# Optimization experiments

Measured on AMD Instinct MI355X. Metric: run time of the kernel, lower is better.

## Reference

```python
import jax, jax.numpy as jnp
import numpy as np
from jax import lax

B = 16           # graphs per batch
N_PER = 4096     # points per graph (equal-sized graphs)
C_IN = 32        # in_channels
RATIO = 0.25
MAX_NBR = 32     # max_num_neighbors in radius()


def _xavier(key, fan_in, fan_out):
    lim = np.sqrt(6.0 / (fan_in + fan_out)).astype(np.float32)
    return jax.random.uniform(key, (fan_in, fan_out), jnp.float32, -lim, lim)


def setup_inputs() -> dict:
    key = jax.random.key(0)
    ks = jax.random.split(key, 16)
    x = jax.random.normal(ks[0], (B * N_PER, C_IN), jnp.float32)
    pos = jax.random.uniform(ks[1], (B * N_PER, 3), jnp.float32) * 20.0
    batch = jnp.repeat(jnp.arange(B, dtype=jnp.int64), N_PER)
    p = {
        'x': x, 'pos': pos, 'batch': batch,
        'scaler_mean': jnp.zeros((1, C_IN), jnp.float32),
        'scaler_std': jnp.ones((1, C_IN), jnp.float32),
        # SA1: Linear(32+3,64) -> Sigmoid -> Linear(64,128)
        'sa1_w1': _xavier(ks[2], C_IN + 3, 64), 'sa1_b1': jnp.zeros((64,), jnp.float32),
        'sa1_w2': _xavier(ks[3], 64, 128),      'sa1_b2': jnp.zeros((128,), jnp.float32),
        # SA2: Linear(128+3,128) -> Sigmoid -> Linear(128,256)
        'sa2_w1': _xavier(ks[4], 128 + 3, 128), 'sa2_b1': jnp.zeros((128,), jnp.float32),
        'sa2_w2': _xavier(ks[5], 128, 256),     'sa2_b2': jnp.zeros((256,), jnp.float32),
        # Global SA: Linear(256+3,256) -> Sigmoid -> Linear(256,512)
        'g_w1': _xavier(ks[6], 256 + 3, 256),   'g_b1': jnp.zeros((256,), jnp.float32),
        'g_w2': _xavier(ks[7], 256, 512),       'g_b2': jnp.zeros((512,), jnp.float32),
        # fc: Linear(512,256) -> Sigmoid -> Linear(256,128)
        'fc_w1': _xavier(ks[8], 512, 256),      'fc_b1': jnp.zeros((256,), jnp.float32),
        'fc_w2': _xavier(ks[9], 256, 128),      'fc_b2': jnp.zeros((128,), jnp.float32),
    }
    return p


def _fps(pos, k):
    # Farthest point sampling, deterministic start at index 0. pos: [B, n, 3] -> idx [B, k]
    pos = lax.stop_gradient(pos)
    d0 = jnp.sum((pos - pos[:, :1, :]) ** 2, -1)  # [B, n] dist^2 to start point

    def step(mind, _):
        nxt = jnp.argmax(mind, axis=1)                                  # [B]
        p = jnp.take_along_axis(pos, nxt[:, None, None], axis=1)        # [B,1,3]
        mind = jnp.minimum(mind, jnp.sum((pos - p) ** 2, -1))
        return mind, nxt

    _, rest = lax.scan(step, d0, None, length=k - 1)                    # [k-1, B]
    start = jnp.zeros((1, pos.shape[0]), rest.dtype)
    return jnp.concatenate([start, rest], 0).T                          # [B, k]


def _gather_nbr(v, nbr):
    # v: [B, n, C], nbr: [B, k, MAX_NBR] -> [B, k, MAX_NBR, C]
    return jax.vmap(lambda vb, nb: vb[nb])(v, nbr)


def _sa_module(x, pos, w1, b1, w2, b2, ratio, r):
    # PointNetConv (max aggregation) over a radius graph from FPS centers.
    Bb, n, _ = x.shape
    k = int(n * ratio)
    idx = _fps(pos, k)                                                  # [B, k]
    pos_dst = jnp.take_along_axis(pos, idx[:, :, None], axis=1)         # [B, k, 3]
    d2 = jnp.sum((pos_dst[:, :, None, :] - pos[:, None, :, :]) ** 2, -1)  # [B,k,n]
    masked = jnp.where(d2 <= r * r, d2, jnp.inf)
    negv, nbr = lax.top_k(-masked, MAX_NBR)                             # nearest <=32 within radius
    valid = jnp.isfinite(negv)                                          # [B,k,32]
    x_j = _gather_nbr(x, nbr)                                           # [B,k,32,C]
    rel = _gather_nbr(pos, nbr) - pos_dst[:, :, None, :]                # pos_j - pos_i
    feat = jnp.concatenate([x_j, rel], axis=-1)
    msg = jax.nn.sigmoid(feat @ w1 + b1) @ w2 + b2                      # [B,k,32,2h]
    msg = jnp.where(valid[..., None], msg, -jnp.inf)
    agg = jnp.max(msg, axis=2)                                          # max aggregation
    agg = jnp.where(jnp.isfinite(agg), agg, 0.0)  # (self is always a neighbor, defensive)
    return jax.nn.relu(agg), pos_dst


def reference(x, pos, batch, scaler_mean, scaler_std,
              sa1_w1, sa1_b1, sa1_w2, sa1_b2,
              sa2_w1, sa2_b1, sa2_w2, sa2_b2,
              g_w1, g_b1, g_w2, g_b2,
              fc_w1, fc_b1, fc_w2, fc_b2):
    x = (x - scaler_mean) / scaler_std
    xb = x.reshape(B, N_PER, -1)      # batch is sorted with N_PER points per graph
    pb = pos.reshape(B, N_PER, 3)
    xb, pb = _sa_module(xb, pb, sa1_w1, sa1_b1, sa1_w2, sa1_b2, RATIO, 2.0)
    xb, pb = _sa_module(xb, pb, sa2_w1, sa2_b1, sa2_w2, sa2_b2, RATIO, 4.0)
    # GlobalSAModule: relu(nn(cat[x, pos])) then global max pool
    h = jnp.concatenate([xb, pb], axis=-1)
    h = jax.nn.relu(jax.nn.sigmoid(h @ g_w1 + g_b1) @ g_w2 + g_b2)      # [B, 256, 512]
    g = jnp.max(h, axis=1)                                              # [B, 512]
    out = jax.nn.sigmoid(g @ fc_w1 + fc_b1) @ fc_w2 + fc_b2
    return jax.nn.relu(out)                                             # last_act='relu'
```

## Files before the change

kernel.cpp:

```cpp
#include <hip/hip_runtime.h>
#include <hip/hip_bf16.h>
#include <math.h>

namespace {

constexpr int NB   = 16;
constexpr int N1   = 4096;
constexpr int K1   = 1024;
constexpr int K2   = 256;
constexpr int MAXN = 32;

__device__ __forceinline__ float sigmoidf_(float x) {
  return 1.0f / (1.0f + __expf(-x));
}

__device__ __forceinline__ float readlane_f(float v, int l) {
  return __int_as_float(__builtin_amdgcn_readlane(__float_as_int(v), l));
}


#define FPS_DPP_STEP(CTRL)                                                     \
  {                                                                            \
    const unsigned olo =                                                       \
        (unsigned)__builtin_amdgcn_update_dpp(0, (int)lo, (CTRL), 0xF, 0xF, true); \
    const unsigned ohi =                                                       \
        (unsigned)__builtin_amdgcn_update_dpp(0, (int)hi, (CTRL), 0xF, 0xF, true); \
    const unsigned long long o = ((unsigned long long)ohi << 32) | olo;        \
    const unsigned long long cur = ((unsigned long long)hi << 32) | lo;        \
    if (o > cur) { lo = olo; hi = ohi; }                                       \
  }

template<int NPT>
__device__ __forceinline__ void fps_level(
    const float* __restrict__ sx, const float* __restrict__ sy,
    const float* __restrict__ sz, int k,
    float* __restrict__ selx, float* __restrict__ sely,
    float* __restrict__ selz,
    unsigned long long (*red)[4]) {
  const int t = threadIdx.x;
  const int lane = t & 63, wave = t >> 6;
  float px[NPT], py[NPT], pz[NPT], mind[NPT];
  unsigned niv[NPT];
  const float c0x = sx[0], c0y = sy[0], c0z = sz[0];
  unsigned long long best = 0;
#pragma unroll
  for (int i = 0; i < NPT; i++) {
    const int p = i * 256 + t;
    niv[i] = ~(unsigned)p;
    px[i] = sx[p]; py[i] = sy[p]; pz[i] = sz[p];
    const float dx = px[i] - c0x, dy = py[i] - c0y, dz = pz[i] - c0z;
    const float d2 = dx * dx + dy * dy + dz * dz;
    mind[i] = d2;
    const unsigned long long cand =
        ((unsigned long long)__float_as_uint(d2) << 32) | niv[i];
    if (cand > best) best = cand;
  }
  if (t == 0) { selx[0] = c0x; sely[0] = c0y; selz[0] = c0z; }
  for (int it = 1; it < k; it++) {
    unsigned lo = (unsigned)best, hi = (unsigned)(best >> 32);
    FPS_DPP_STEP(0x111)
    FPS_DPP_STEP(0x112)
    FPS_DPP_STEP(0x114)
    FPS_DPP_STEP(0x118)
    FPS_DPP_STEP(0x142)
    FPS_DPP_STEP(0x143)
    const int par = it & 1;
    if (lane == 63) red[par][wave] = ((unsigned long long)hi << 32) | lo;
    __syncthreads();
    const unsigned long long w0 = red[par][0], w1 = red[par][1];
    const unsigned long long w2 = red[par][2], w3 = red[par][3];
    const unsigned long long m01 = w0 > w1 ? w0 : w1;
    const unsigned long long m23 = w2 > w3 ? w2 : w3;
    const unsigned long long win = m01 > m23 ? m01 : m23;
    const int p = (int)(~(unsigned)win);
    const float nx = sx[p], ny = sy[p], nz = sz[p];
    if (t == 0) { selx[it] = nx; sely[it] = ny; selz[it] = nz; }
    best = 0;
#pragma unroll
    for (int i = 0; i < NPT; i++) {
      const float dx = px[i] - nx, dy = py[i] - ny, dz = pz[i] - nz;
      const float d2 = dx * dx + dy * dy + dz * dz;
      const float m = fminf(mind[i], d2);
      mind[i] = m;
      const unsigned long long cand =
          ((unsigned long long)__float_as_uint(m) << 32) | niv[i];
      if (cand > best) best = cand;
    }
  }
}

#undef FPS_DPP_STEP

__global__ __launch_bounds__(256) void fps_fused_kernel(
    const float* __restrict__ pos, float* __restrict__ posd1,
    float* __restrict__ posd2, unsigned int* __restrict__ gout) {
  __shared__ float sx[N1], sy[N1], sz[N1];
  __shared__ float s2x[K1], s2y[K1], s2z[K1];
  __shared__ float p2x[K2], p2y[K2], p2z[K2];
  __shared__ __align__(16) unsigned long long red[2][4];
  const int b = blockIdx.x;
  const int t = threadIdx.x;
  gout[b * 512 + t] = 0u;
  gout[b * 512 + t + 256] = 0u;
  const float* pb = pos + (size_t)b * N1 * 3;
  for (int p = t; p < N1; p += 256) {
    sx[p] = pb[p * 3 + 0]; sy[p] = pb[p * 3 + 1]; sz[p] = pb[p * 3 + 2];
  }
  __syncthreads();
  fps_level<N1 / 256>(sx, sy, sz, K1, s2x, s2y, s2z, red);
  __syncthreads();
  fps_level<K1 / 256>(s2x, s2y, s2z, K2, p2x, p2y, p2z, red);
  __syncthreads();
  float* o1 = posd1 + (size_t)b * K1 * 3;
  for (int i = t; i < K1; i += 256) {
    o1[i * 3 + 0] = s2x[i]; o1[i * 3 + 1] = s2y[i]; o1[i * 3 + 2] = s2z[i];
  }
  float* o2 = posd2 + (size_t)b * K2 * 3;
  for (int i = t; i < K2; i += 256) {
    o2[i * 3 + 0] = p2x[i]; o2[i * 3 + 1] = p2y[i]; o2[i * 3 + 2] = p2z[i];
  }
}

template<int N, int CAP>
__global__ __launch_bounds__(256) void radius_nbr_kernel(
    const float* __restrict__ pts, const float* __restrict__ ctr,
    int K, float r2, int* __restrict__ nbr, int* __restrict__ cnt_out) {
  __shared__ float candd[4][CAP];
  __shared__ int   candi[4][CAP];
  const int t = threadIdx.x;
  const int lane = t & 63, wave = t >> 6;
  const int bpg = K / 4;
  const int b = blockIdx.x / bpg;
  const int ci = (blockIdx.x % bpg) * 4 + wave;
  const float* pb = pts + (size_t)b * N * 3;
  const size_t cbase = ((size_t)b * K + ci) * 3;
  const float cx = ctr[cbase + 0], cy = ctr[cbase + 1], cz = ctr[cbase + 2];
  int total = 0;
  for (int base = 0; base < N; base += 64) {
    const int p = base + lane;
    const float dx = pb[p * 3 + 0] - cx;
    const float dy = pb[p * 3 + 1] - cy;
    const float dz = pb[p * 3 + 2] - cz;
    const float d2 = dx * dx + dy * dy + dz * dz;
    const bool pred = d2 <= r2;
    const unsigned long long m = __ballot(pred);
    if (pred) {
      const int slot = total + __popcll(m & ((1ull << lane) - 1ull));
      if (slot < CAP) { candd[wave][slot] = d2; candi[wave][slot] = p; }
    }
    total += __popcll(m);
  }
  if (total > CAP) total = CAP;
  int* nbp = nbr + ((size_t)b * K + ci) * MAXN;
  if (total <= MAXN) {
    if (lane < total) nbp[lane] = candi[wave][lane];
  } else {
    for (int jj = 0; jj < MAXN; jj++) {
      float bvd = INFINITY; int bvi = 0x7fffffff; int bslot = 0;
      for (int s = lane; s < total; s += 64) {
        const float d = candd[wave][s];
        const int i = candi[wave][s];
        if (d < bvd || (d == bvd && i < bvi)) { bvd = d; bvi = i; bslot = s; }
      }
#pragma unroll
      for (int off = 32; off; off >>= 1) {
        const float od = __shfl_xor(bvd, off);
        const int   oi = __shfl_xor(bvi, off);
        const int   os = __shfl_xor(bslot, off);
        if (od < bvd || (od == bvd && oi < bvi)) { bvd = od; bvi = oi; bslot = os; }
      }
      if (lane == 0) { nbp[jj] = bvi; candd[wave][bslot] = INFINITY; }
    }
  }
  if (lane == 0) cnt_out[(size_t)b * K + ci] = (total < MAXN) ? total : MAXN;
}

template<int CIN_T, int H, int COUT, bool SCALE>
__global__ __launch_bounds__(256) void sa_conv_kernel(
    const float* __restrict__ xin, const float* __restrict__ pts,
    const float* __restrict__ ctr, const int* __restrict__ nbr,
    const int* __restrict__ cnt,
    const float* __restrict__ w1, const float* __restrict__ b1,
    const float* __restrict__ w2, const float* __restrict__ b2,
    const float* __restrict__ smean, const float* __restrict__ sstd,
    int N, int K, float* __restrict__ xout) {
  constexpr int FIN  = CIN_T + 3;
  constexpr int KREG = (FIN + 63) / 64;
  constexpr int HREG = H / 64;
  constexpr int CREG = COUT / 64;
  constexpr int RPW  = MAXN / 4;
  __shared__ float part[4][COUT];
  const int t = threadIdx.x, lane = t & 63, wave = t >> 6;
  const int bk = blockIdx.x;
  const int b = bk / K;
  const int V = cnt[bk];
  float m[CREG];
#pragma unroll
  for (int ck = 0; ck < CREG; ck++) m[ck] = -INFINITY;
  if (V > wave * RPW) {
    const int* nb = nbr + (size_t)bk * MAXN;
    const float ctrx = ctr[(size_t)bk * 3 + 0];
    const float ctry = ctr[(size_t)bk * 3 + 1];
    const float ctrz = ctr[(size_t)bk * 3 + 2];
    float sm = 0.0f, sd = 1.0f;
    if (SCALE && lane < CIN_T) { sm = smean[lane]; sd = sstd[lane]; }
    float fr[RPW][KREG];
#pragma unroll
    for (int r = 0; r < RPW; r++) {
      const int j = wave * RPW + r;
      const int p = (j < V) ? nb[j] : nb[0];
#pragma unroll
      for (int k2 = 0; k2 < KREG; k2++) {
        const int f = k2 * 64 + lane;
        float v = 0.0f;
        if (f < CIN_T) {
          v = xin[((size_t)b * N + p) * CIN_T + f];
          if constexpr (SCALE) v = (v - sm) / sd;
        } else if (f < FIN) {
          const int d = f - CIN_T;
          const float pv = pts[((size_t)b * N + p) * 3 + d];
          v = pv - (d == 0 ? ctrx : (d == 1 ? ctry : ctrz));
        }
        fr[r][k2] = v;
      }
    }
    float hh[RPW][HREG];
    {
      float acc[RPW][HREG];
#pragma unroll
      for (int r = 0; r < RPW; r++)
#pragma unroll
        for (int hk = 0; hk < HREG; hk++) acc[r][hk] = 0.0f;
#pragma unroll
      for (int k2 = 0; k2 < KREG; k2++) {
        const int lim = (FIN - k2 * 64) < 64 ? (FIN - k2 * 64) : 64;
        for (int fl = 0; fl < lim; fl++) {
          const int f = k2 * 64 + fl;
          float wv[HREG];
#pragma unroll
          for (int hk = 0; hk < HREG; hk++) wv[hk] = w1[(size_t)f * H + hk * 64 + lane];
#pragma unroll
          for (int r = 0; r < RPW; r++) {
            const float s = readlane_f(fr[r][k2], fl);
#pragma unroll
            for (int hk = 0; hk < HREG; hk++) acc[r][hk] = fmaf(s, wv[hk], acc[r][hk]);
          }
        }
      }
#pragma unroll
      for (int hk = 0; hk < HREG; hk++) {
        const float bb = b1[hk * 64 + lane];
#pragma unroll
        for (int r = 0; r < RPW; r++) hh[r][hk] = sigmoidf_(acc[r][hk] + bb);
      }
    }
    float acc2[RPW][CREG];
#pragma unroll
    for (int r = 0; r < RPW; r++)
#pragma unroll
      for (int ck = 0; ck < CREG; ck++) acc2[r][ck] = 0.0f;
#pragma unroll
    for (int hk = 0; hk < HREG; hk++) {
      for (int hl = 0; hl < 64; hl++) {
        const int h = hk * 64 + hl;
        float wv[CREG];
#pragma unroll
        for (int ck = 0; ck < CREG; ck++) wv[ck] = w2[(size_t)h * COUT + ck * 64 + lane];
#pragma unroll
        for (int r = 0; r < RPW; r++) {
          const float s = readlane_f(hh[r][hk], hl);
#pragma unroll
          for (int ck = 0; ck < CREG; ck++) acc2[r][ck] = fmaf(s, wv[ck], acc2[r][ck]);
        }
      }
    }
#pragma unroll
    for (int r = 0; r < RPW; r++) {
      if (wave * RPW + r < V) {
#pragma unroll
        for (int ck = 0; ck < CREG; ck++) m[ck] = fmaxf(m[ck], acc2[r][ck]);
      }
    }
  }
#pragma unroll
  for (int ck = 0; ck < CREG; ck++) part[wave][ck * 64 + lane] = m[ck];
  __syncthreads();
  if (t < COUT) {
    const float mm = fmaxf(fmaxf(part[0][t], part[1][t]),
                           fmaxf(part[2][t], part[3][t]));
    const float o = mm + b2[t];
    xout[(size_t)bk * COUT + t] = o > 0.0f ? o : 0.0f;
  }
}

__global__ __launch_bounds__(256) void global_sa_kernel(
    const float* __restrict__ x2, const float* __restrict__ posd2,
    const float* __restrict__ gw1, const float* __restrict__ gb1,
    const float* __restrict__ gw2, const float* __restrict__ gb2,
    unsigned int* __restrict__ gout) {
  __shared__ float fin[4][259];
  __shared__ float s[4][256];
  const int t = threadIdx.x;
  const int blk = blockIdx.x;
  const int b = blk / 64;
  const int p0 = (blk % 64) * 4;
  for (int item = t; item < 4 * 259; item += 256) {
    const int p = item / 259, f = item - p * 259;
    const float v = (f < 256)
        ? x2[((size_t)b * 256 + p0 + p) * 256 + f]
        : posd2[((size_t)b * 256 + p0 + p) * 3 + (f - 256)];
    fin[p][f] = v;
  }
  __syncthreads();
  float acc[4] = {0.f, 0.f, 0.f, 0.f};
  for (int f = 0; f < 259; f++) {
    const float w = gw1[f * 256 + t];
#pragma unroll
    for (int p = 0; p < 4; p++) acc[p] = fmaf(fin[p][f], w, acc[p]);
  }
  const float bb = gb1[t];
#pragma unroll
  for (int p = 0; p < 4; p++) s[p][t] = sigmoidf_(acc[p] + bb);
  __syncthreads();
  float a0[4] = {0.f, 0.f, 0.f, 0.f}, a1[4] = {0.f, 0.f, 0.f, 0.f};
  for (int h = 0; h < 256; h++) {
    const float w0 = gw2[h * 512 + t];
    const float w1v = gw2[h * 512 + t + 256];
#pragma unroll
    for (int p = 0; p < 4; p++) {
      a0[p] = fmaf(s[p][h], w0, a0[p]);
      a1[p] = fmaf(s[p][h], w1v, a1[p]);
    }
  }
  const float b0 = gb2[t], b1v = gb2[t + 256];
  float m0 = 0.0f, m1 = 0.0f;
#pragma unroll
  for (int p = 0; p < 4; p++) {
    m0 = fmaxf(m0, fmaxf(a0[p] + b0, 0.0f));
    m1 = fmaxf(m1, fmaxf(a1[p] + b1v, 0.0f));
  }
  atomicMax(&gout[b * 512 + t], __float_as_uint(m0));
  atomicMax(&gout[b * 512 + t + 256], __float_as_uint(m1));
}

__global__ __launch_bounds__(256) void fc_kernel(
    const unsigned int* __restrict__ g,
    const float* __restrict__ fw1, const float* __restrict__ fb1,
    const float* __restrict__ fw2, const float* __restrict__ fb2,
    float* __restrict__ out) {
  __shared__ float gv[512];
  __shared__ float s[256];
  const int b = blockIdx.x, t = threadIdx.x;
  gv[t] = __uint_as_float(g[b * 512 + t]);
  gv[t + 256] = __uint_as_float(g[b * 512 + t + 256]);
  __syncthreads();
  float acc = 0.0f;
  for (int h = 0; h < 512; h++) acc = fmaf(gv[h], fw1[h * 256 + t], acc);
  s[t] = sigmoidf_(acc + fb1[t]);
  __syncthreads();
  if (t < 128) {
    float a2 = 0.0f;
    for (int h = 0; h < 256; h++) a2 = fmaf(s[h], fw2[h * 128 + t], a2);
    const float o = a2 + fb2[t];
    out[b * 128 + t] = o > 0.0f ? o : 0.0f;
  }
}

}

extern "C" void kernel_launch(void* const* d_in, const int* in_sizes, int n_in,
                              void* d_out, int out_size, void* d_ws, size_t ws_size,
                              hipStream_t stream) {
  (void)in_sizes; (void)n_in; (void)out_size; (void)ws_size;
  const float* x     = (const float*)d_in[0];
  const float* pos   = (const float*)d_in[1];
  const float* smean = (const float*)d_in[3];
  const float* sstd  = (const float*)d_in[4];
  const float* s1w1  = (const float*)d_in[5];
  const float* s1b1  = (const float*)d_in[6];
  const float* s1w2  = (const float*)d_in[7];
  const float* s1b2  = (const float*)d_in[8];
  const float* s2w1  = (const float*)d_in[9];
  const float* s2b1  = (const float*)d_in[10];
  const float* s2w2  = (const float*)d_in[11];
  const float* s2b2  = (const float*)d_in[12];
  const float* gw1   = (const float*)d_in[13];
  const float* gb1   = (const float*)d_in[14];
  const float* gw2   = (const float*)d_in[15];
  const float* gb2   = (const float*)d_in[16];
  const float* fw1   = (const float*)d_in[17];
  const float* fb1   = (const float*)d_in[18];
  const float* fw2   = (const float*)d_in[19];
  const float* fb2   = (const float*)d_in[20];

  char* ws = (char*)d_ws;
  size_t off = 0;
  auto take = [&](size_t bytes) -> char* {
    char* p = ws + off;
    off = (off + bytes + 255) & ~(size_t)255;
    return p;
  };
  float* posd1       = (float*)take((size_t)NB * K1 * 3 * 4);
  int*   nbr1        = (int*)take((size_t)NB * K1 * MAXN * 4);
  int*   cnt1        = (int*)take((size_t)NB * K1 * 4);
  float* x1          = (float*)take((size_t)NB * K1 * 128 * 4);
  float* posd2       = (float*)take((size_t)NB * K2 * 3 * 4);
  int*   nbr2        = (int*)take((size_t)NB * K2 * MAXN * 4);
  int*   cnt2        = (int*)take((size_t)NB * K2 * 4);
  float* x2          = (float*)take((size_t)NB * K2 * 256 * 4);
  unsigned int* gbuf = (unsigned int*)take((size_t)NB * 512 * 4);

  hipLaunchKernelGGL(fps_fused_kernel, dim3(NB), dim3(256), 0, stream,
                     pos, posd1, posd2, gbuf);
  hipLaunchKernelGGL((radius_nbr_kernel<N1, 448>), dim3(NB * K1 / 4), dim3(256), 0, stream,
                     pos, posd1, K1, 4.0f, nbr1, cnt1);
  hipLaunchKernelGGL((sa_conv_kernel<32, 64, 128, true>), dim3(NB * K1), dim3(256), 0, stream,
                     x, pos, posd1, nbr1, cnt1, s1w1, s1b1, s1w2, s1b2,
                     smean, sstd, N1, K1, x1);
  hipLaunchKernelGGL((radius_nbr_kernel<K1, 448>), dim3(NB * K2 / 4), dim3(256), 0, stream,
                     posd1, posd2, K2, 16.0f, nbr2, cnt2);
  hipLaunchKernelGGL((sa_conv_kernel<128, 128, 256, false>), dim3(NB * K2), dim3(256), 0, stream,
                     x1, posd1, posd2, nbr2, cnt2, s2w1, s2b1, s2w2, s2b2,
                     nullptr, nullptr, K1, K2, x2);
  hipLaunchKernelGGL(global_sa_kernel, dim3(NB * 64), dim3(256), 0, stream,
                     x2, posd2, gw1, gb1, gw2, gb2, gbuf);
  hipLaunchKernelGGL(fc_kernel, dim3(NB), dim3(256), 0, stream,
                     gbuf, fw1, fb1, fw2, fb2, (float*)d_out);
}
```

Baseline: 1.275 ms.

## Split FPS levels and co-schedule independent stages in merged heterogeneous kernels

Second-level farthest point sampling moves out of the single-block-per-graph FPS kernel into a merged kernel that also runs the level-1 radius search, so the serial FPS runs alongside the radius blocks. Likewise, the level-2 radius search and the level-1 SA conv share one launch, since neither depends on the other. The SA conv weight loads also change to vectorized float2/float4 with an interleaved channel mapping per lane. The aim is to hide the long-latency, 16-block serial FPS behind parallel work and cut launch gaps. The cost is larger shared-memory footprints on the merged kernels, which may lower occupancy.

```diff
diff --git a/kernel.cpp b/kernel.cpp
--- a/kernel.cpp
+++ b/kernel.cpp
@@ -9,6 +9,7 @@
 constexpr int K1   = 1024;
 constexpr int K2   = 256;
 constexpr int MAXN = 32;
+constexpr int RCAP = 448;
 
 __device__ __forceinline__ float sigmoidf_(float x) {
   return 1.0f / (1.0f + __expf(-x));
@@ -91,12 +92,11 @@
 
 #undef FPS_DPP_STEP
 
-__global__ __launch_bounds__(256) void fps_fused_kernel(
+__global__ __launch_bounds__(256) void fps_l1_kernel(
     const float* __restrict__ pos, float* __restrict__ posd1,
-    float* __restrict__ posd2, unsigned int* __restrict__ gout) {
+    unsigned int* __restrict__ gout) {
   __shared__ float sx[N1], sy[N1], sz[N1];
   __shared__ float s2x[K1], s2y[K1], s2z[K1];
-  __shared__ float p2x[K2], p2y[K2], p2z[K2];
   __shared__ __align__(16) unsigned long long red[2][4];
   const int b = blockIdx.x;
   const int t = threadIdx.x;
@@ -109,29 +109,32 @@
   __syncthreads();
   fps_level<N1 / 256>(sx, sy, sz, K1, s2x, s2y, s2z, red);
   __syncthreads();
-  fps_level<K1 / 256>(s2x, s2y, s2z, K2, p2x, p2y, p2z, red);
-  __syncthreads();
   float* o1 = posd1 + (size_t)b * K1 * 3;
   for (int i = t; i < K1; i += 256) {
     o1[i * 3 + 0] = s2x[i]; o1[i * 3 + 1] = s2y[i]; o1[i * 3 + 2] = s2z[i];
   }
-  float* o2 = posd2 + (size_t)b * K2 * 3;
-  for (int i = t; i < K2; i += 256) {
-    o2[i * 3 + 0] = p2x[i]; o2[i * 3 + 1] = p2y[i]; o2[i * 3 + 2] = p2z[i];
-  }
-}
-
-template<int N, int CAP>
-__global__ __launch_bounds__(256) void radius_nbr_kernel(
+}
+
+struct FpsL2Smem {
+  float s2x[K1], s2y[K1], s2z[K1];
+  float p2x[K2], p2y[K2], p2z[K2];
+  unsigned long long red[2][4];
+};
+struct RadSmem {
+  float candd[4][RCAP];
+  int   candi[4][RCAP];
+};
+
+template<int N>
+__device__ __forceinline__ void radius_body(
     const float* __restrict__ pts, const float* __restrict__ ctr,
-    int K, float r2, int* __restrict__ nbr, int* __restrict__ cnt_out) {
-  __shared__ float candd[4][CAP];
-  __shared__ int   candi[4][CAP];
+    int K, float r2, int* __restrict__ nbr, int* __restrict__ cnt_out,
+    RadSmem& sm, int rb) {
   const int t = threadIdx.x;
   const int lane = t & 63, wave = t >> 6;
   const int bpg = K / 4;
-  const int b = blockIdx.x / bpg;
-  const int ci = (blockIdx.x % bpg) * 4 + wave;
+  const int b = rb / bpg;
+  const int ci = (rb % bpg) * 4 + wave;
   const float* pb = pts + (size_t)b * N * 3;
   const size_t cbase = ((size_t)b * K + ci) * 3;
   const float cx = ctr[cbase + 0], cy = ctr[cbase + 1], cz = ctr[cbase + 2];
@@ -146,20 +149,20 @@
     const unsigned long long m = __ballot(pred);
     if (pred) {
       const int slot = total + __popcll(m & ((1ull << lane) - 1ull));
-      if (slot < CAP) { candd[wave][slot] = d2; candi[wave][slot] = p; }
+      if (slot < RCAP) { sm.candd[wave][slot] = d2; sm.candi[wave][slot] = p; }
     }
     total += __popcll(m);
   }
-  if (total > CAP) total = CAP;
+  if (total > RCAP) total = RCAP;
   int* nbp = nbr + ((size_t)b * K + ci) * MAXN;
   if (total <= MAXN) {
-    if (lane < total) nbp[lane] = candi[wave][lane];
+    if (lane < total) nbp[lane] = sm.candi[wave][lane];
   } else {
     for (int jj = 0; jj < MAXN; jj++) {
       float bvd = INFINITY; int bvi = 0x7fffffff; int bslot = 0;
       for (int s = lane; s < total; s += 64) {
-        const float d = candd[wave][s];
-        const int i = candi[wave][s];
+        const float d = sm.candd[wave][s];
+        const int i = sm.candi[wave][s];
         if (d < bvd || (d == bvd && i < bvi)) { bvd = d; bvi = i; bslot = s; }
       }
 #pragma unroll
@@ -169,29 +172,56 @@
         const int   os = __shfl_xor(bslot, off);
         if (od < bvd || (od == bvd && oi < bvi)) { bvd = od; bvi = oi; bslot = os; }
       }
-      if (lane == 0) { nbp[jj] = bvi; candd[wave][bslot] = INFINITY; }
+      if (lane == 0) { nbp[jj] = bvi; sm.candd[wave][bslot] = INFINITY; }
     }
   }
   if (lane == 0) cnt_out[(size_t)b * K + ci] = (total < MAXN) ? total : MAXN;
 }
 
+__global__ __launch_bounds__(256) void l2_radius1_kernel(
+    const float* __restrict__ pos, const float* __restrict__ posd1,
+    float* __restrict__ posd2, int* __restrict__ nbr1,
+    int* __restrict__ cnt1) {
+  constexpr size_t SMB =
+      sizeof(FpsL2Smem) > sizeof(RadSmem) ? sizeof(FpsL2Smem) : sizeof(RadSmem);
+  __shared__ __align__(16) char smem[SMB];
+  const int t = threadIdx.x;
+  if (blockIdx.x < (unsigned)NB) {
+    FpsL2Smem& f = *reinterpret_cast<FpsL2Smem*>(smem);
+    const int b = blockIdx.x;
+    const float* p1 = posd1 + (size_t)b * K1 * 3;
+    for (int i = t; i < K1; i += 256) {
+      f.s2x[i] = p1[i * 3 + 0]; f.s2y[i] = p1[i * 3 + 1]; f.s2z[i] = p1[i * 3 + 2];
+    }
+    __syncthreads();
+    fps_level<K1 / 256>(f.s2x, f.s2y, f.s2z, K2, f.p2x, f.p2y, f.p2z, f.red);
+    __syncthreads();
+    float* o2 = posd2 + (size_t)b * K2 * 3;
+    for (int i = t; i < K2; i += 256) {
+      o2[i * 3 + 0] = f.p2x[i]; o2[i * 3 + 1] = f.p2y[i]; o2[i * 3 + 2] = f.p2z[i];
+    }
+  } else {
+    RadSmem& r = *reinterpret_cast<RadSmem*>(smem);
+    radius_body<N1>(pos, posd1, K1, 4.0f, nbr1, cnt1, r, blockIdx.x - NB);
+  }
+}
+
 template<int CIN_T, int H, int COUT, bool SCALE>
-__global__ __launch_bounds__(256) void sa_conv_kernel(
+__device__ __forceinline__ void sa_conv_body(
     const float* __restrict__ xin, const float* __restrict__ pts,
     const float* __restrict__ ctr, const int* __restrict__ nbr,
     const int* __restrict__ cnt,
     const float* __restrict__ w1, const float* __restrict__ b1,
     const float* __restrict__ w2, const float* __restrict__ b2,
     const float* __restrict__ smean, const float* __restrict__ sstd,
-    int N, int K, float* __restrict__ xout) {
+    int N, int K, float* __restrict__ xout, float* part ,
+    int bk) {
   constexpr int FIN  = CIN_T + 3;
   constexpr int KREG = (FIN + 63) / 64;
   constexpr int HREG = H / 64;
   constexpr int CREG = COUT / 64;
   constexpr int RPW  = MAXN / 4;
-  __shared__ float part[4][COUT];
   const int t = threadIdx.x, lane = t & 63, wave = t >> 6;
-  const int bk = blockIdx.x;
   const int b = bk / K;
   const int V = cnt[bk];
   float m[CREG];
@@ -230,47 +260,59 @@
 #pragma unroll
       for (int r = 0; r < RPW; r++)
 #pragma unroll
-        for (int hk = 0; hk < HREG; hk++) acc[r][hk] = 0.0f;
+        for (int q = 0; q < HREG; q++) acc[r][q] = 0.0f;
 #pragma unroll
       for (int k2 = 0; k2 < KREG; k2++) {
         const int lim = (FIN - k2 * 64) < 64 ? (FIN - k2 * 64) : 64;
         for (int fl = 0; fl < lim; fl++) {
           const int f = k2 * 64 + fl;
           float wv[HREG];
-#pragma unroll
-          for (int hk = 0; hk < HREG; hk++) wv[hk] = w1[(size_t)f * H + hk * 64 + lane];
+          if constexpr (HREG == 1) {
+            wv[0] = w1[(size_t)f * H + lane];
+          } else {
+            const float2 w = *reinterpret_cast<const float2*>(
+                &w1[(size_t)f * H + lane * 2]);
+            wv[0] = w.x; wv[1] = w.y;
+          }
 #pragma unroll
           for (int r = 0; r < RPW; r++) {
             const float s = readlane_f(fr[r][k2], fl);
 #pragma unroll
-            for (int hk = 0; hk < HREG; hk++) acc[r][hk] = fmaf(s, wv[hk], acc[r][hk]);
+            for (int q = 0; q < HREG; q++) acc[r][q] = fmaf(s, wv[q], acc[r][q]);
           }
         }
       }
 #pragma unroll
-      for (int hk = 0; hk < HREG; hk++) {
-        const float bb = b1[hk * 64 + lane];
-#pragma unroll
-        for (int r = 0; r < RPW; r++) hh[r][hk] = sigmoidf_(acc[r][hk] + bb);
+      for (int q = 0; q < HREG; q++) {
+        const float bb = b1[lane * HREG + q];
+#pragma unroll
+        for (int r = 0; r < RPW; r++) hh[r][q] = sigmoidf_(acc[r][q] + bb);
       }
     }
     float acc2[RPW][CREG];
 #pragma unroll
     for (int r = 0; r < RPW; r++)
 #pragma unroll
-      for (int ck = 0; ck < CREG; ck++) acc2[r][ck] = 0.0f;
-#pragma unroll
-    for (int hk = 0; hk < HREG; hk++) {
-      for (int hl = 0; hl < 64; hl++) {
-        const int h = hk * 64 + hl;
+      for (int q = 0; q < CREG; q++) acc2[r][q] = 0.0f;
+    for (int hl = 0; hl < 64; hl++) {
+#pragma unroll
+      for (int q1 = 0; q1 < HREG; q1++) {
+        const int h = hl * HREG + q1;
         float wv[CREG];
-#pragma unroll
-        for (int ck = 0; ck < CREG; ck++) wv[ck] = w2[(size_t)h * COUT + ck * 64 + lane];
+        if constexpr (CREG == 2) {
+          const float2 w = *reinterpret_cast<const float2*>(
+              &w2[(size_t)h * COUT + lane * 2]);
+          wv[0] = w.x; wv[1] = w.y;
+        } else {
+          const float4 w = *reinterpret_cast<const float4*>(
+              &w2[(size_t)h * COUT + lane * 4]);
+          wv[0] = w.x; wv[1] = w.y; wv[2] = w.z; wv[3] = w.w;
+        }
 #pragma unroll
         for (int r = 0; r < RPW; r++) {
-          const float s = readlane_f(hh[r][hk], hl);
-#pragma unroll
-          for (int ck = 0; ck < CREG; ck++) acc2[r][ck] = fmaf(s, wv[ck], acc2[r][ck]);
+          const float s = readlane_f(hh[r][q1], hl);
+#pragma unroll
+          for (int q = 0; q < CREG; q++) acc2[r][q] = fmaf(s, wv[q], acc2[r][q]);
         }
       }
     }
@@ -278,19 +320,57 @@
     for (int r = 0; r < RPW; r++) {
       if (wave * RPW + r < V) {
 #pragma unroll
-        for (int ck = 0; ck < CREG; ck++) m[ck] = fmaxf(m[ck], acc2[r][ck]);
-      }
-    }
-  }
-#pragma unroll
-  for (int ck = 0; ck < CREG; ck++) part[wave][ck * 64 + lane] = m[ck];
+        for (int q = 0; q < CREG; q++) m[q] = fmaxf(m[q], acc2[r][q]);
+      }
+    }
+  }
+#pragma unroll
+  for (int q = 0; q < CREG; q++) part[wave * COUT + lane * CREG + q] = m[q];
   __syncthreads();
   if (t < COUT) {
-    const float mm = fmaxf(fmaxf(part[0][t], part[1][t]),
-                           fmaxf(part[2][t], part[3][t]));
+    const float mm = fmaxf(fmaxf(part[0 * COUT + t], part[1 * COUT + t]),
+                           fmaxf(part[2 * COUT + t], part[3 * COUT + t]));
     const float o = mm + b2[t];
     xout[(size_t)bk * COUT + t] = o > 0.0f ? o : 0.0f;
   }
+}
+
+__global__ __launch_bounds__(256) void rad2_conv1_kernel(
+    const float* __restrict__ posd1, const float* __restrict__ posd2,
+    int* __restrict__ nbr2, int* __restrict__ cnt2,
+    const float* __restrict__ x, const float* __restrict__ pos,
+    const int* __restrict__ nbr1, const int* __restrict__ cnt1,
+    const float* __restrict__ s1w1, const float* __restrict__ s1b1,
+    const float* __restrict__ s1w2, const float* __restrict__ s1b2,
+    const float* __restrict__ smean, const float* __restrict__ sstd,
+    float* __restrict__ x1) {
+  constexpr int NRAD = NB * K2 / 4;
+  constexpr size_t SMB =
+      sizeof(RadSmem) > sizeof(float) * 4 * 128 ? sizeof(RadSmem)
+                                                : sizeof(float) * 4 * 128;
+  __shared__ __align__(16) char smem[SMB];
+  if (blockIdx.x < (unsigned)NRAD) {
+    RadSmem& r = *reinterpret_cast<RadSmem*>(smem);
+    radius_body<K1>(posd1, posd2, K2, 16.0f, nbr2, cnt2, r, blockIdx.x);
+  } else {
+    float* part = reinterpret_cast<float*>(smem);
+    sa_conv_body<32, 64, 128, true>(x, pos, posd1, nbr1, cnt1,
+                                    s1w1, s1b1, s1w2, s1b2, smean, sstd,
+                                    N1, K1, x1, part, blockIdx.x - NRAD);
+  }
+}
+
+__global__ __launch_bounds__(256) void conv2_kernel(
+    const float* __restrict__ x1, const float* __restrict__ posd1,
+    const float* __restrict__ posd2, const int* __restrict__ nbr2,
+    const int* __restrict__ cnt2,
+    const float* __restrict__ s2w1, const float* __restrict__ s2b1,
+    const float* __restrict__ s2w2, const float* __restrict__ s2b2,
+    float* __restrict__ x2) {
+  __shared__ __align__(16) float part[4 * 256];
+  sa_conv_body<128, 128, 256, false>(x1, posd1, posd2, nbr2, cnt2,
+                                     s2w1, s2b1, s2w2, s2b2, nullptr, nullptr,
+                                     K1, K2, x2, part, blockIdx.x);
 }
 
 __global__ __launch_bounds__(256) void global_sa_kernel(
@@ -410,18 +490,15 @@
   float* x2          = (float*)take((size_t)NB * K2 * 256 * 4);
   unsigned int* gbuf = (unsigned int*)take((size_t)NB * 512 * 4);
 
-  hipLaunchKernelGGL(fps_fused_kernel, dim3(NB), dim3(256), 0, stream,
-                     pos, posd1, posd2, gbuf);
-  hipLaunchKernelGGL((radius_nbr_kernel<N1, 448>), dim3(NB * K1 / 4), dim3(256), 0, stream,
-                     pos, posd1, K1, 4.0f, nbr1, cnt1);
-  hipLaunchKernelGGL((sa_conv_kernel<32, 64, 128, true>), dim3(NB * K1), dim3(256), 0, stream,
-                     x, pos, posd1, nbr1, cnt1, s1w1, s1b1, s1w2, s1b2,
-                     smean, sstd, N1, K1, x1);
-  hipLaunchKernelGGL((radius_nbr_kernel<K1, 448>), dim3(NB * K2 / 4), dim3(256), 0, stream,
-                     posd1, posd2, K2, 16.0f, nbr2, cnt2);
-  hipLaunchKernelGGL((sa_conv_kernel<128, 128, 256, false>), dim3(NB * K2), dim3(256), 0, stream,
-                     x1, posd1, posd2, nbr2, cnt2, s2w1, s2b1, s2w2, s2b2,
-                     nullptr, nullptr, K1, K2, x2);
+  hipLaunchKernelGGL(fps_l1_kernel, dim3(NB), dim3(256), 0, stream,
+                     pos, posd1, gbuf);
+  hipLaunchKernelGGL(l2_radius1_kernel, dim3(NB + NB * K1 / 4), dim3(256), 0, stream,
+                     pos, posd1, posd2, nbr1, cnt1);
+  hipLaunchKernelGGL(rad2_conv1_kernel, dim3(NB * K2 / 4 + NB * K1), dim3(256), 0, stream,
+                     posd1, posd2, nbr2, cnt2, x, pos, nbr1, cnt1,
+                     s1w1, s1b1, s1w2, s1b2, smean, sstd, x1);
+  hipLaunchKernelGGL(conv2_kernel, dim3(NB * K2), dim3(256), 0, stream,
+                     x1, posd1, posd2, nbr2, cnt2, s2w1, s2b1, s2w2, s2b2, x2);
   hipLaunchKernelGGL(global_sa_kernel, dim3(NB * 64), dim3(256), 0, stream,
                      x2, posd2, gw1, gb1, gw2, gb2, gbuf);
   hipLaunchKernelGGL(fc_kernel, dim3(NB), dim3(256), 0, stream,
```

After: 1.182 ms. 7.3% less time.
